# Kernel optimization log

Hardware: AMD Instinct MI355X
Metric: run time of the kernel (lower is better)

Reference implementation:

```python
import jax, jax.numpy as jnp
import numpy as np

VOCAB = 50257
EMBED_DIM = 1024
FRONT_DIM = 2048  # int(embed_dim * front_embed_mul)
BATCH, SEQ = 4, 4096


def setup_inputs() -> dict:
    key = jax.random.key(0)
    k_idx, k_emb, k_w1, k_b1, k_w2, k_b2 = jax.random.split(key, 6)
    idxs = jax.random.randint(k_idx, (BATCH, SEQ), 0, VOCAB, dtype=jnp.int64)
    tok_embed = jax.random.normal(k_emb, (VOCAB, FRONT_DIM), dtype=jnp.float32)
    # torch nn.Linear weights are [out, in]
    W1 = jax.random.normal(k_w1, (EMBED_DIM, FRONT_DIM), dtype=jnp.float32) * (1.0 / np.sqrt(FRONT_DIM))
    b1 = jax.random.normal(k_b1, (EMBED_DIM,), dtype=jnp.float32) * 0.01
    W2 = jax.random.normal(k_w2, (EMBED_DIM, EMBED_DIM), dtype=jnp.float32) * (1.0 / np.sqrt(EMBED_DIM))
    b2 = jax.random.normal(k_b2, (EMBED_DIM,), dtype=jnp.float32) * 0.01
    return {"idxs": idxs, "tok_embed": tok_embed, "W1": W1, "b1": b1, "W2": W2, "b2": b2}


def reference(idxs, tok_embed, W1, b1, W2, b2):
    # Embedding gather: [B, S, front_dim]
    x = tok_embed[idxs]
    # integration1: Linear(front_dim -> embed_dim)
    x = jnp.einsum('bsf,ef->bse', x, W1) + b1
    # exact (erf-based) GELU, matching torch F.gelu default
    x = jax.nn.gelu(x, approximate=False)
    # integration2: Linear(embed_dim -> embed_dim)
    x = jnp.einsum('bse,oe->bso', x, W2) + b2
    return x
```

## Files before the change

kernel.cpp:

```cpp
#include <hip/hip_runtime.h>
#include <hip/hip_bf16.h>

typedef __attribute__((ext_vector_type(4))) float floatx4;
typedef __attribute__((ext_vector_type(8))) short short8;
typedef __attribute__((ext_vector_type(8))) unsigned short ushortx8;

#define K1 2048
#define N1 1024
#define K2 1024
#define N2 1024

__device__ __forceinline__ unsigned short f2bf(float f) {
  __hip_bfloat16 h = __float2bfloat16(f);
  return __builtin_bit_cast(unsigned short, h);
}

__device__ __forceinline__ void gload_lds16(const void* g, void* l) {
  __builtin_amdgcn_global_load_lds(
      (__attribute__((address_space(1))) void*)const_cast<void*>(g),
      (__attribute__((address_space(3))) void*)l, 16, 0, 0);
}

__global__ __launch_bounds__(256) void cvt2_kernel(
    const float* __restrict__ W1, const float* __restrict__ W2,
    unsigned short* __restrict__ W1b, unsigned short* __restrict__ W2b) {
  int i = blockIdx.x * blockDim.x + threadIdx.x;
  const float* src;
  unsigned short* dst;
  if (i < 524288) {
    src = (const float*)&reinterpret_cast<const float4*>(W1)[i];
    dst = (unsigned short*)&reinterpret_cast<ushort4*>(W1b)[i];
  } else {
    int k = i - 524288;
    if (k >= 262144) return;
    src = (const float*)&reinterpret_cast<const float4*>(W2)[k];
    dst = (unsigned short*)&reinterpret_cast<ushort4*>(W2b)[k];
  }
  float4 f = *reinterpret_cast<const float4*>(src);
  ushort4 o;
  o.x = f2bf(f.x); o.y = f2bf(f.y); o.z = f2bf(f.z); o.w = f2bf(f.w);
  *reinterpret_cast<ushort4*>(dst) = o;
}

__global__ __launch_bounds__(512, 2) void gemm1_fused_kernel(
    const int* __restrict__ idxs, const float* __restrict__ tok,
    const unsigned short* __restrict__ W1b, const float* __restrict__ b1,
    unsigned short* __restrict__ hout) {
  __shared__ unsigned short S[65536];
  const int t = threadIdx.x;
  const int p = blockIdx.x;
  const int bid = (p & 7) * 32 + (p >> 3);
  const int bm = bid >> 2, bn = bid & 3;
  const int brow0 = bm * 256, bcol0 = bn * 256;
  const int lane = t & 63, w = t >> 6;
  const int wm = w >> 2, wn = w & 3;
  const int fr = lane & 15, kg2 = lane >> 4;

  const int srow = t >> 3;
  const int cg = (t & 7) ^ (srow & 7);
  const float* aqf[4];
  const unsigned short* bq[4];
#pragma unroll
  for (int q = 0; q < 4; ++q) {
    const int ridx = idxs[brow0 + srow + 64 * q];
    aqf[q] = tok + (size_t)ridx * K1 + cg * 8;
    bq[q] = W1b + (size_t)(bcol0 + srow + 64 * q) * K1 + cg * 8;
  }
  const int t8 = t * 8;

  floatx4 acc[8][4] = {};
  constexpr int NT = K1 / 64;

  float4 av[4][2];
  auto loadA = [&](int k0) {
#pragma unroll
    for (int q = 0; q < 4; ++q) {
      av[q][0] = *reinterpret_cast<const float4*>(aqf[q] + k0);
      av[q][1] = *reinterpret_cast<const float4*>(aqf[q] + k0 + 4);
    }
  };
  auto writeA = [&](int d) {
#pragma unroll
    for (int q = 0; q < 4; ++q) {
      ushortx8 u;
      u[0] = f2bf(av[q][0].x); u[1] = f2bf(av[q][0].y);
      u[2] = f2bf(av[q][0].z); u[3] = f2bf(av[q][0].w);
      u[4] = f2bf(av[q][1].x); u[5] = f2bf(av[q][1].y);
      u[6] = f2bf(av[q][1].z); u[7] = f2bf(av[q][1].w);
      *reinterpret_cast<ushortx8*>(&S[d * 16384 + t8 + q * 4096]) = u;
    }
  };
  auto issueB = [&](int d, int k0) {
#pragma unroll
    for (int q = 0; q < 4; ++q)
      gload_lds16(bq[q] + k0, &S[32768 + d * 16384 + t8 + q * 4096]);
  };
  auto computeKS = [&](int cur, int ks) {
    const int sl = ((ks * 4 + kg2) ^ (fr & 7)) * 8;
    short8 bf[4];
#pragma unroll
    for (int j = 0; j < 4; ++j)
      bf[j] = *(const short8*)&S[32768 + cur * 16384 + (wn * 64 + j * 16 + fr) * 64 + sl];
    __builtin_amdgcn_s_setprio(1);
#pragma unroll
    for (int i = 0; i < 8; ++i) {
      const short8 af = *(const short8*)&S[cur * 16384 + (wm * 128 + i * 16 + fr) * 64 + sl];
#pragma unroll
      for (int j = 0; j < 4; ++j)
        acc[i][j] = __builtin_amdgcn_mfma_f32_16x16x32_bf16(af, bf[j], acc[i][j], 0, 0, 0);
    }
    __builtin_amdgcn_s_setprio(0);
  };

  loadA(0);
  issueB(0, 0);
  writeA(0);
  asm volatile("s_waitcnt vmcnt(0) lgkmcnt(0)\ns_barrier" ::: "memory");

#pragma unroll 1
  for (int tt = 0; tt < NT; ++tt) {
    const int cur = tt & 1;
    const int nbuf = cur ^ 1;
    const bool pf = (tt + 1 < NT);
    const int nk = (tt + 1) * 64;
    if (pf) {
      loadA(nk);
      issueB(nbuf, nk);
    }
    computeKS(cur, 0);
    if (pf) writeA(nbuf);
    computeKS(cur, 1);
    asm volatile("s_waitcnt vmcnt(0) lgkmcnt(0)\ns_barrier" ::: "memory");
  }

  const int ec0 = bcol0 + wn * 64 + fr;
  float bv[4];
#pragma unroll
  for (int j = 0; j < 4; ++j) bv[j] = b1[ec0 + j * 16];
  unsigned short* Wl = S + w * 8192;
#pragma unroll
  for (int i = 0; i < 8; ++i)
#pragma unroll
    for (int j = 0; j < 4; ++j)
#pragma unroll
      for (int r = 0; r < 4; ++r) {
        float v = acc[i][j][r] + bv[j];
        v = 0.5f * v * (1.0f + erff(v * 0.70710678118654752f));
        const int row = i * 16 + kg2 * 4 + r;
        const int col = (j * 16 + fr) ^ (kg2 << 3);
        Wl[row * 64 + col] = f2bf(v);
      }
  asm volatile("s_waitcnt lgkmcnt(0)" ::: "memory");
#pragma unroll
  for (int pass = 0; pass < 16; ++pass) {
    const int wr = pass * 8 + (lane >> 3);
    const int ch = (lane & 7) ^ ((wr >> 2) & 3);
    const short8 v8 = *(const short8*)&Wl[wr * 64 + ch * 8];
    *reinterpret_cast<short8*>(
        &hout[(size_t)(brow0 + wm * 128 + wr) * N1 + bcol0 + wn * 64 + (lane & 7) * 8]) = v8;
  }
}

__global__ __launch_bounds__(512, 2) void gemm2_kernel(
    const unsigned short* __restrict__ A, const unsigned short* __restrict__ Bw,
    const float* __restrict__ bias, float* __restrict__ out) {
  __shared__ unsigned short S[65536];
  const int t = threadIdx.x;
  const int p = blockIdx.x;
  const int bid = (p & 7) * 32 + (p >> 3);
  const int bm = bid >> 2, bn = bid & 3;
  const int brow0 = bm * 256, bcol0 = bn * 256;
  const int lane = t & 63, w = t >> 6;
  const int wm = w >> 2, wn = w & 3;
  const int fr = lane & 15, kg2 = lane >> 4;

  const int srow = t >> 3;
  const int cg = (t & 7) ^ (srow & 7);
  const unsigned short* aq[4];
  const unsigned short* bq[4];
#pragma unroll
  for (int q = 0; q < 4; ++q) {
    aq[q] = A + (size_t)(brow0 + srow + 64 * q) * K2 + cg * 8;
    bq[q] = Bw + (size_t)(bcol0 + srow + 64 * q) * K2 + cg * 8;
  }
  const int t8 = t * 8;

  floatx4 acc[8][4] = {};
  constexpr int NT = K2 / 64;

  auto stage = [&](int d, int k0) {
#pragma unroll
    for (int q = 0; q < 4; ++q) {
      gload_lds16(aq[q] + k0, &S[d * 16384 + t8 + q * 4096]);
      gload_lds16(bq[q] + k0, &S[32768 + d * 16384 + t8 + q * 4096]);
    }
  };
  auto compute = [&](int cur) {
#pragma unroll
    for (int ks = 0; ks < 2; ++ks) {
      const int sl = ((ks * 4 + kg2) ^ (fr & 7)) * 8;
      short8 bf[4];
#pragma unroll
      for (int j = 0; j < 4; ++j)
        bf[j] = *(const short8*)&S[32768 + cur * 16384 + (wn * 64 + j * 16 + fr) * 64 + sl];
      __builtin_amdgcn_s_setprio(1);
#pragma unroll
      for (int i = 0; i < 8; ++i) {
        const short8 af = *(const short8*)&S[cur * 16384 + (wm * 128 + i * 16 + fr) * 64 + sl];
#pragma unroll
        for (int j = 0; j < 4; ++j)
          acc[i][j] = __builtin_amdgcn_mfma_f32_16x16x32_bf16(af, bf[j], acc[i][j], 0, 0, 0);
      }
      __builtin_amdgcn_s_setprio(0);
    }
  };

  stage(0, 0);
#pragma unroll 1
  for (int it = 0; it < NT - 1; ++it) {
    const int cur = it & 1;
    stage(cur ^ 1, (it + 1) * 64);
    asm volatile("s_waitcnt vmcnt(8)\ns_barrier" ::: "memory");
    compute(cur);
    asm volatile("s_waitcnt lgkmcnt(0)\ns_barrier" ::: "memory");
  }
  asm volatile("s_waitcnt vmcnt(0)\ns_barrier" ::: "memory");
  compute((NT - 1) & 1);
  asm volatile("s_waitcnt lgkmcnt(0)\ns_barrier" ::: "memory");

  const int ec0 = bcol0 + wn * 64 + fr;
  float bv[4];
#pragma unroll
  for (int j = 0; j < 4; ++j) bv[j] = bias[ec0 + j * 16];
  float* Wf = reinterpret_cast<float*>(S) + w * 4096;
#pragma unroll
  for (int ih = 0; ih < 2; ++ih) {
#pragma unroll
    for (int i4 = 0; i4 < 4; ++i4)
#pragma unroll
      for (int j = 0; j < 4; ++j)
#pragma unroll
        for (int r = 0; r < 4; ++r) {
          const int row = i4 * 16 + kg2 * 4 + r;
          const int col = (j * 16 + fr) ^ (kg2 << 2);
          Wf[row * 64 + col] = acc[ih * 4 + i4][j][r] + bv[j];
        }
    asm volatile("s_waitcnt lgkmcnt(0)" ::: "memory");
#pragma unroll
    for (int pass = 0; pass < 16; ++pass) {
      const int wr = pass * 4 + (lane >> 4);
      const int ch = (lane & 15) ^ ((wr >> 2) & 3);
      const floatx4 v4 = *(const floatx4*)&Wf[wr * 64 + ch * 4];
      *reinterpret_cast<floatx4*>(
          &out[(size_t)(brow0 + wm * 128 + ih * 64 + wr) * N2 + bcol0 + wn * 64 +
               (lane & 15) * 4]) = v4;
    }
    if (ih == 0)
      asm volatile("s_waitcnt lgkmcnt(0)" ::: "memory");
  }
}

extern "C" void kernel_launch(void* const* d_in, const int* in_sizes, int n_in,
                              void* d_out, int out_size, void* d_ws, size_t ws_size,
                              hipStream_t stream) {
  const int* idxs = (const int*)d_in[0];
  const float* tok = (const float*)d_in[1];
  const float* W1 = (const float*)d_in[2];
  const float* b1 = (const float*)d_in[3];
  const float* W2 = (const float*)d_in[4];
  const float* b2 = (const float*)d_in[5];
  float* out = (float*)d_out;

  unsigned short* W1b = (unsigned short*)d_ws;
  unsigned short* W2b = (unsigned short*)((char*)d_ws + (4u << 20));
  unsigned short* hbuf = (unsigned short*)((char*)d_ws + (6u << 20));

  cvt2_kernel<<<3072, 256, 0, stream>>>(W1, W2, W1b, W2b);
  gemm1_fused_kernel<<<256, 512, 0, stream>>>(idxs, tok, W1b, b1, hbuf);
  gemm2_kernel<<<256, 512, 0, stream>>>(hbuf, W2b, b2, out);
}
```

Baseline: 140.9 us.

## Restructure GEMM2 main loop into half-K-tile stages with interleaved loads

Rewrites the second GEMM's K-loop so each 64-wide K tile is split into two 32-wide halves with a new LDS layout and XOR swizzle. Global-to-LDS loads for the next halves are issued between smaller MFMA groups of 16, with explicit barriers and vmcnt waits, so memory traffic is spread across the compute phases. The aim is finer-grained overlap of loads with MFMAs, at the cost of more barriers per iteration.

Result: slower. 144.8 us (+2.8%).

```diff
diff --git a/kernel.cpp b/kernel.cpp
--- a/kernel.cpp
+++ b/kernel.cpp
@@ -174,60 +174,103 @@
   const int wm = w >> 2, wn = w & 3;
   const int fr = lane & 15, kg2 = lane >> 4;
 
-  const int srow = t >> 3;
-  const int cg = (t & 7) ^ (srow & 7);
-  const unsigned short* aq[4];
-  const unsigned short* bq[4];
-#pragma unroll
-  for (int q = 0; q < 4; ++q) {
-    aq[q] = A + (size_t)(brow0 + srow + 64 * q) * K2 + cg * 8;
-    bq[q] = Bw + (size_t)(bcol0 + srow + 64 * q) * K2 + cg * 8;
-  }
+  const int srow4 = t >> 2;
+  const int cgk = (t & 3) ^ ((t >> 3) & 3);
+  const unsigned short* aP0 = A + (size_t)(brow0 + srow4) * K2 + cgk * 8;
+  const unsigned short* aP1 = A + (size_t)(brow0 + srow4 + 128) * K2 + cgk * 8;
+  const unsigned short* bP0 = Bw + (size_t)(bcol0 + srow4) * K2 + cgk * 8;
+  const unsigned short* bP1 = Bw + (size_t)(bcol0 + srow4 + 128) * K2 + cgk * 8;
   const int t8 = t * 8;
+
+  const int slA = (kg2 ^ ((fr >> 1) & 3)) * 8;
+  const int aO = wm * 4096 + fr * 32 + slA;
+  const int bO = (wn >> 1) * 4096 + ((wn & 1) * 64 + fr) * 32 + slA;
 
   floatx4 acc[8][4] = {};
   constexpr int NT = K2 / 64;
 
-  auto stage = [&](int d, int k0) {
-#pragma unroll
-    for (int q = 0; q < 4; ++q) {
-      gload_lds16(aq[q] + k0, &S[d * 16384 + t8 + q * 4096]);
-      gload_lds16(bq[q] + k0, &S[32768 + d * 16384 + t8 + q * 4096]);
-    }
-  };
-  auto compute = [&](int cur) {
-#pragma unroll
-    for (int ks = 0; ks < 2; ++ks) {
-      const int sl = ((ks * 4 + kg2) ^ (fr & 7)) * 8;
-      short8 bf[4];
-#pragma unroll
-      for (int j = 0; j < 4; ++j)
-        bf[j] = *(const short8*)&S[32768 + cur * 16384 + (wn * 64 + j * 16 + fr) * 64 + sl];
-      __builtin_amdgcn_s_setprio(1);
-#pragma unroll
-      for (int i = 0; i < 8; ++i) {
-        const short8 af = *(const short8*)&S[cur * 16384 + (wm * 128 + i * 16 + fr) * 64 + sl];
-#pragma unroll
-        for (int j = 0; j < 4; ++j)
-          acc[i][j] = __builtin_amdgcn_mfma_f32_16x16x32_bf16(af, bf[j], acc[i][j], 0, 0, 0);
-      }
-      __builtin_amdgcn_s_setprio(0);
-    }
-  };
-
-  stage(0, 0);
+#define ISSA(buf, tt_, kh)                                                    \
+  do {                                                                        \
+    gload_lds16(aP0 + (tt_)*64 + (kh)*32, &S[(buf)*16384 + (kh)*8192 + t8]);  \
+    gload_lds16(aP1 + (tt_)*64 + (kh)*32,                                     \
+                &S[(buf)*16384 + (kh)*8192 + 4096 + t8]);                     \
+  } while (0)
+#define ISSB(buf, tt_, kh)                                                    \
+  do {                                                                        \
+    gload_lds16(bP0 + (tt_)*64 + (kh)*32,                                     \
+                &S[32768 + (buf)*16384 + (kh)*8192 + t8]);                    \
+    gload_lds16(bP1 + (tt_)*64 + (kh)*32,                                     \
+                &S[32768 + (buf)*16384 + (kh)*8192 + 4096 + t8]);             \
+  } while (0)
+#define RD_B(buf, kh)                                                         \
+  do {                                                                        \
+    _Pragma("unroll") for (int j = 0; j < 4; ++j)                             \
+        bf[j] = *(const short8*)&S[32768 + (buf)*16384 + (kh)*8192 + bO + j * 512]; \
+  } while (0)
+#define RD_A(buf, kh, IH)                                                     \
+  do {                                                                        \
+    _Pragma("unroll") for (int ii = 0; ii < 4; ++ii)                          \
+        af[ii] = *(const short8*)&S[(buf)*16384 + (kh)*8192 + aO + ((IH)*4 + ii) * 512]; \
+  } while (0)
+#define MF16(IH)                                                              \
+  do {                                                                        \
+    __builtin_amdgcn_s_setprio(1);                                            \
+    _Pragma("unroll") for (int ii = 0; ii < 4; ++ii)                          \
+        _Pragma("unroll") for (int j = 0; j < 4; ++j)                         \
+            acc[(IH)*4 + ii][j] = __builtin_amdgcn_mfma_f32_16x16x32_bf16(    \
+                af[ii], bf[j], acc[(IH)*4 + ii][j], 0, 0, 0);                 \
+    __builtin_amdgcn_s_setprio(0);                                            \
+  } while (0)
+#define BAR asm volatile("s_barrier" ::: "memory")
+#define LGKM0 asm volatile("s_waitcnt lgkmcnt(0)" ::: "memory")
+
+  ISSA(0, 0, 0); ISSB(0, 0, 0);
+  ISSA(0, 0, 1); ISSB(0, 0, 1);
+  ISSA(1, 1, 0); ISSB(1, 1, 0);
+  asm volatile("s_waitcnt vmcnt(4)" ::: "memory");
+  BAR;
+
+  short8 af[4], bf[4];
 #pragma unroll 1
-  for (int it = 0; it < NT - 1; ++it) {
-    const int cur = it & 1;
-    stage(cur ^ 1, (it + 1) * 64);
-    asm volatile("s_waitcnt vmcnt(8)\ns_barrier" ::: "memory");
-    compute(cur);
-    asm volatile("s_waitcnt lgkmcnt(0)\ns_barrier" ::: "memory");
-  }
-  asm volatile("s_waitcnt vmcnt(0)\ns_barrier" ::: "memory");
-  compute((NT - 1) & 1);
+  for (int tt = 0; tt < NT; ++tt) {
+    const int p_ = tt & 1, q_ = p_ ^ 1;
+    const bool i1 = (tt + 1 < NT), i2 = (tt + 2 < NT);
+    RD_B(p_, 0);
+    RD_A(p_, 0, 0);
+    if (i1) ISSA(q_, tt + 1, 1);
+    BAR; LGKM0;
+    MF16(0);
+    BAR;
+    RD_A(p_, 0, 1);
+    if (i1) ISSB(q_, tt + 1, 1);
+    BAR; LGKM0;
+    MF16(1);
+    BAR;
+    RD_B(p_, 1);
+    RD_A(p_, 1, 0);
+    if (i2) ISSA(p_, tt + 2, 0);
+    BAR; LGKM0;
+    MF16(0);
+    BAR;
+    RD_A(p_, 1, 1);
+    if (i2) ISSB(p_, tt + 2, 0);
+    BAR; LGKM0;
+    MF16(1);
+    if (i1) {
+      if (i2) asm volatile("s_waitcnt vmcnt(4)" ::: "memory");
+      else    asm volatile("s_waitcnt vmcnt(0)" ::: "memory");
+    }
+    BAR;
+  }
+#undef ISSA
+#undef ISSB
+#undef RD_A
+#undef RD_B
+#undef MF16
+#undef BAR
+#undef LGKM0
+
   asm volatile("s_waitcnt lgkmcnt(0)\ns_barrier" ::: "memory");
-
   const int ec0 = bcol0 + wn * 64 + fr;
   float bv[4];
 #pragma unroll
```

## Prefetch gathered A rows two K-tiles ahead with register double buffering

Applied to the files above, without the earlier changes.

The first GEMM's main loop now holds the fp32 embedding rows in two register buffers and issues the gather loads two K-tiles ahead, while the B tiles still go straight to LDS one tile ahead. The loop is unrolled by two so the LDS buffer indices are fixed, and the end-of-step barrier waits with vmcnt(8), which lets the outstanding A loads stay in flight across the barrier. The goal is to hide the latency of the random-row gather behind more MFMA work. The cost is another 32 VGPRs for the second buffer, which may reduce occupancy, and the scheme depends on the vmcnt count matching the order in which loads are issued.

New measurement: 392.2 us. +178.3%, slower.

```diff
diff --git a/kernel.cpp b/kernel.cpp
--- a/kernel.cpp
+++ b/kernel.cpp
@@ -71,22 +71,22 @@
   floatx4 acc[8][4] = {};
   constexpr int NT = K1 / 64;
 
-  float4 av[4][2];
-  auto loadA = [&](int k0) {
+  float4 avA[4][2], avB[4][2];
+  auto loadTo = [&](float4 (&dst)[4][2], int k0) {
 #pragma unroll
     for (int q = 0; q < 4; ++q) {
-      av[q][0] = *reinterpret_cast<const float4*>(aqf[q] + k0);
-      av[q][1] = *reinterpret_cast<const float4*>(aqf[q] + k0 + 4);
-    }
-  };
-  auto writeA = [&](int d) {
+      dst[q][0] = *reinterpret_cast<const float4*>(aqf[q] + k0);
+      dst[q][1] = *reinterpret_cast<const float4*>(aqf[q] + k0 + 4);
+    }
+  };
+  auto writeAv = [&](int d, const float4 (&src)[4][2]) {
 #pragma unroll
     for (int q = 0; q < 4; ++q) {
       ushortx8 u;
-      u[0] = f2bf(av[q][0].x); u[1] = f2bf(av[q][0].y);
-      u[2] = f2bf(av[q][0].z); u[3] = f2bf(av[q][0].w);
-      u[4] = f2bf(av[q][1].x); u[5] = f2bf(av[q][1].y);
-      u[6] = f2bf(av[q][1].z); u[7] = f2bf(av[q][1].w);
+      u[0] = f2bf(src[q][0].x); u[1] = f2bf(src[q][0].y);
+      u[2] = f2bf(src[q][0].z); u[3] = f2bf(src[q][0].w);
+      u[4] = f2bf(src[q][1].x); u[5] = f2bf(src[q][1].y);
+      u[6] = f2bf(src[q][1].z); u[7] = f2bf(src[q][1].w);
       *reinterpret_cast<ushortx8*>(&S[d * 16384 + t8 + q * 4096]) = u;
     }
   };
@@ -112,25 +112,44 @@
     __builtin_amdgcn_s_setprio(0);
   };
 
-  loadA(0);
-  issueB(0, 0);
-  writeA(0);
-  asm volatile("s_waitcnt vmcnt(0) lgkmcnt(0)\ns_barrier" ::: "memory");
+  {
+    float4 tv[4][2];
+    loadTo(tv, 0);
+    issueB(0, 0);
+    loadTo(avB, 64);
+    writeAv(0, tv);
+    asm volatile("s_waitcnt vmcnt(0) lgkmcnt(0)\ns_barrier" ::: "memory");
+  }
 
 #pragma unroll 1
-  for (int tt = 0; tt < NT; ++tt) {
-    const int cur = tt & 1;
-    const int nbuf = cur ^ 1;
-    const bool pf = (tt + 1 < NT);
-    const int nk = (tt + 1) * 64;
-    if (pf) {
-      loadA(nk);
-      issueB(nbuf, nk);
-    }
-    computeKS(cur, 0);
-    if (pf) writeA(nbuf);
-    computeKS(cur, 1);
-    asm volatile("s_waitcnt vmcnt(0) lgkmcnt(0)\ns_barrier" ::: "memory");
+  for (int t2 = 0; t2 < NT; t2 += 2) {
+    {
+      const int tt = t2;
+      const bool pf2 = (tt + 2 < NT);
+      issueB(1, (tt + 1) * 64);
+      computeKS(0, 0);
+      writeAv(1, avB);
+      if (pf2) loadTo(avA, (tt + 2) * 64);
+      computeKS(0, 1);
+      if (pf2)
+        asm volatile("s_waitcnt vmcnt(8) lgkmcnt(0)\ns_barrier" ::: "memory");
+      else
+        asm volatile("s_waitcnt vmcnt(0) lgkmcnt(0)\ns_barrier" ::: "memory");
+    }
+    {
+      const int tt = t2 + 1;
+      const bool pf = (tt + 1 < NT);
+      const bool pf2 = (tt + 2 < NT);
+      if (pf) issueB(0, (tt + 1) * 64);
+      computeKS(1, 0);
+      if (pf) writeAv(0, avA);
+      if (pf2) loadTo(avB, (tt + 2) * 64);
+      computeKS(1, 1);
+      if (pf2)
+        asm volatile("s_waitcnt vmcnt(8) lgkmcnt(0)\ns_barrier" ::: "memory");
+      else
+        asm volatile("s_waitcnt vmcnt(0) lgkmcnt(0)\ns_barrier" ::: "memory");
+    }
   }
 
   const int ec0 = bcol0 + wn * 64 + fr;
```
